# Kernel optimization log

Hardware: AMD Instinct MI355X
Metric: run time of the kernel (lower is better)

## Reference

```python
import jax, jax.numpy as jnp
import numpy as np

NUM_ROUTERS = 8
K = 2
IN_DIM = 384
HID = 64
TEMP = 1.0
AUX_COEF = 0.05
EPS = 1e-12


def _l2norm(v, axis=-1):
    n = jnp.sqrt(jnp.sum(v * v, axis=axis, keepdims=True))
    return v / jnp.maximum(n, EPS)


def setup_inputs() -> dict:
    key = jax.random.key(0)
    ks = jax.random.split(key, 10)
    B, E = 8192, 1024
    s = 1.0 / np.sqrt(IN_DIM)
    return {
        "x": jax.random.normal(ks[0], (B, IN_DIM), jnp.float32),
        "reasoning_embeddings": jax.random.normal(ks[1], (E, IN_DIM), jnp.float32),
        "random_num": jax.random.uniform(ks[2], (B, 1), jnp.float32),
        "gate_w": jax.random.normal(ks[3], (IN_DIM, NUM_ROUTERS), jnp.float32) * s,
        "gate_b": jnp.zeros((NUM_ROUTERS,), jnp.float32),
        "Uw": jax.random.normal(ks[4], (NUM_ROUTERS, IN_DIM, HID), jnp.float32) * s,
        "Ub": jnp.zeros((NUM_ROUTERS, HID), jnp.float32),
        "Vw": jax.random.normal(ks[5], (NUM_ROUTERS, IN_DIM, HID), jnp.float32) * s,
        "Vb": jnp.zeros((NUM_ROUTERS, HID), jnp.float32),
    }


def reference(x, reasoning_embeddings, random_num, gate_w, gate_b, Uw, Ub, Vw, Vb):
    B = x.shape[0]
    # gate
    logits = x @ gate_w + gate_b                              # [B, R]
    probs = jax.nn.softmax(logits, axis=-1)
    topk_vals, topk_idxs = jax.lax.top_k(logits, K)           # [B, K]
    topk_mask = jax.nn.one_hot(topk_idxs, NUM_ROUTERS).sum(axis=1)  # [B, R]
    aux_loss = NUM_ROUTERS * (probs.mean(0) * topk_mask.mean(0)).sum() * AUX_COEF

    # all routers, batched (replaces the per-(i,j) python loop)
    xu = _l2norm(jnp.einsum("bd,rdh->rbh", x, Uw) + Ub[:, None, :])          # [R, B, H]
    ev = _l2norm(jnp.einsum("ed,rdh->reh", reasoning_embeddings, Vw) + Vb[:, None, :])  # [R, E, H]
    scores = jnp.einsum("rbh,reh->rbe", xu, ev)               # [R, B, E]
    all_out = jax.nn.softmax(scores / TEMP, axis=-1)          # [R, B, E]

    # gather top-k experts per sample
    all_out_b = jnp.transpose(all_out, (1, 0, 2))             # [B, R, E]
    router_outputs = jnp.take_along_axis(all_out_b, topk_idxs[:, :, None], axis=1)  # [B, K, E]

    gate_weights = jax.nn.softmax(topk_vals, axis=-1)[:, :, None]  # [B, K, 1]
    rea_probs = jnp.sum(router_outputs * gate_weights, axis=1)     # [B, E]

    # categorical sampling via inverse-CDF
    scores_cumsum = jnp.cumsum(rea_probs, axis=1)
    selected_index = jnp.argmax((scores_cumsum > random_num).astype(jnp.float32), axis=1)  # [B]
    log_probs = jnp.log(rea_probs[jnp.arange(B), selected_index])[:, None]  # [B, 1]
    return selected_index, log_probs, aux_loss
```

## Files before the change

### kernel.cpp

```cpp
#include <hip/hip_runtime.h>
#include <math.h>

#define B 8192
#define E 1024
#define D 384
#define H 64
#define R 8
#define NCHUNK 16
#define CHUNK_E 64
#define NPOS 16896
#define NROW 25088

#define WS_COUNTS   0u
#define WS_CURSORS  32u
#define WS_PS       64u
#define WS_TOP2     256u
#define WS_GW       65792u
#define WS_POSMAP   131328u
#define WS_LIST     196864u
#define WS_EVN      264448u
#define WS_XUN      2361600u
#define WS_C        6686976u
#define WS_BUFA     7768320u
#define WS_BUFB     14190848u

__global__ __launch_bounds__(256) void k_gate(
    const float* __restrict__ x, const float* __restrict__ gate_w,
    const float* __restrict__ gate_b, int2* __restrict__ top2,
    float2* __restrict__ gwv, int* __restrict__ counts, float* __restrict__ ps)
{
  __shared__ __align__(16) float gwT[R * 388];
  __shared__ float psl[R];
  __shared__ int   cl[R];
  int tid = threadIdx.x;
  for (int idx = tid; idx < D * R; idx += 256) {
    int k = idx >> 3, r = idx & 7;
    gwT[r * 388 + k] = gate_w[idx];
  }
  if (tid < R) { psl[tid] = 0.f; cl[tid] = 0; }
  __syncthreads();

  int l = tid & 63;
  int r = tid & 7;
  int b = blockIdx.x * 32 + (tid >> 3);
  float acc = gate_b[r];
  const float4* x4 = (const float4*)(x + (size_t)b * D);
  const float*  gr = gwT + r * 388;
#pragma unroll 4
  for (int q = 0; q < 96; ++q) {
    float4 xv = x4[q];
    float4 gv = *(const float4*)&gr[q * 4];
    acc = fmaf(xv.x, gv.x, acc);
    acc = fmaf(xv.y, gv.y, acc);
    acc = fmaf(xv.z, gv.z, acc);
    acc = fmaf(xv.w, gv.w, acc);
  }
  float lv[R];
#pragma unroll
  for (int rr = 0; rr < R; ++rr) lv[rr] = __shfl(acc, (l & ~7) + rr);
  int i0 = 0; float v0 = lv[0];
#pragma unroll
  for (int rr = 1; rr < R; ++rr) if (lv[rr] > v0) { v0 = lv[rr]; i0 = rr; }
  int i1 = (i0 == 0) ? 1 : 0; float v1 = lv[i1];
#pragma unroll
  for (int rr = 0; rr < R; ++rr)
    if (rr != i0 && lv[rr] > v1) { v1 = lv[rr]; i1 = rr; }
  float se = 0.f;
#pragma unroll
  for (int rr = 0; rr < R; ++rr) se += expf(lv[rr] - v0);
  float p = expf(acc - v0) / se;
  if (r == 0) {
    float e10 = expf(v1 - v0);
    top2[b] = make_int2(i0, i1);
    gwv[b]  = make_float2(1.f / (1.f + e10), e10 / (1.f + e10));
  }
  float pa = p;
  int   ca = (r == i0 ? 1 : 0) + (r == i1 ? 1 : 0);
#pragma unroll
  for (int m = 8; m < 64; m <<= 1) {
    pa += __shfl_xor(pa, m);
    ca += __shfl_xor(ca, m);
  }
  if (l < 8) { atomicAdd(&psl[r], pa); atomicAdd(&cl[r], ca); }
  __syncthreads();
  if (tid < R) { atomicAdd(&ps[tid], psl[tid]); atomicAdd(&counts[tid], cl[tid]); }
}

__global__ __launch_bounds__(256) void k_scatter(
    const int2* __restrict__ top2, const int* __restrict__ counts,
    const float* __restrict__ ps, int* __restrict__ cursors,
    int* __restrict__ list, int2* __restrict__ posmap, float* __restrict__ out_aux)
{
  __shared__ int lc[R];
  __shared__ int lbase[R];
  __shared__ int offs[R];
  int tid = threadIdx.x;
  if (tid < R) lc[tid] = 0;
  __syncthreads();
  if (tid == 0) {
    int o = 0;
    for (int r2 = 0; r2 < R; ++r2) { offs[r2] = o; o += (min(counts[r2], B) + 63) & ~63; }
  }
  __syncthreads();
  int b = min(blockIdx.x * 256 + tid, B - 1);
  int2 t = top2[b];
  t.x &= 7; t.y &= 7;
  int p0 = atomicAdd(&lc[t.x], 1);
  int p1 = atomicAdd(&lc[t.y], 1);
  __syncthreads();
  if (tid < R) lbase[tid] = atomicAdd(&cursors[tid], lc[tid]);
  __syncthreads();
  int i0 = min(offs[t.x] + lbase[t.x] + p0, NPOS - 1);
  int i1 = min(offs[t.y] + lbase[t.y] + p1, NPOS - 1);
  list[i0] = b * 2 + 0;
  list[i1] = b * 2 + 1;
  posmap[b] = make_int2(i0, i1);
  if (blockIdx.x == 0 && tid == 0) {
    float s = 0.f;
    for (int r2 = 0; r2 < R; ++r2)
      s += (ps[r2] / (float)B) * ((float)min(counts[r2], B) / (float)B);
    out_aux[0] = (float)R * s * 0.05f;
  }
}

__global__ __launch_bounds__(256) void k_projgemm(
    const float* __restrict__ re, const float* __restrict__ x,
    const float* __restrict__ Vw, const float* __restrict__ Uw,
    const int* __restrict__ list, const int* __restrict__ counts,
    float* __restrict__ bufA, float* __restrict__ bufB)
{
  __shared__ __align__(16) float At[64 * 64];
  __shared__ __align__(16) float Wt[64 * 64];
  int tid = threadIdx.x;
  int bid = blockIdx.x;
  int tile = bid >> 1, ks = bid & 1;
  int row0 = tile * 64;

  const float* Wsrc;
  if (row0 < 8192) {
    Wsrc = Vw + (size_t)(row0 >> 10) * (D * H);
  } else {
    int pos0 = row0 - 8192;
    int r = 0, baseq = 0;
    for (int rr = 0; rr < R; ++rr) {
      if (pos0 >= baseq) r = rr;
      baseq += (min(counts[rr], B) + 63) & ~63;
    }
    Wsrc = Uw + (size_t)r * (D * H);
  }

  int srow = tid & 63, sq = tid >> 6;
  const float* arow;
  if (row0 < 8192) {
    arow = re + (size_t)((row0 + srow) & 1023) * D;
  } else {
    int pos = row0 - 8192 + srow;
    int gl = list[min(pos, NPOS - 1)];
    gl = min(max(gl, 0), 2 * B - 1);
    arow = x + (size_t)(gl >> 1) * D;
  }
  int wk = tid >> 2, wc = tid & 3;
  int rg = tid >> 4, hg = tid & 15;

  float acc[4][4];
#pragma unroll
  for (int i = 0; i < 4; ++i)
#pragma unroll
    for (int j = 0; j < 4; ++j) acc[i][j] = 0.f;

  for (int kt = 0; kt < 3; ++kt) {
    int kb = ks * 192 + kt * 64;
    __syncthreads();
#pragma unroll
    for (int q = 0; q < 4; ++q) {
      float4 v = *(const float4*)&arow[kb + sq * 16 + q * 4];
      int k0 = sq * 16 + q * 4;
      At[(k0 + 0) * 64 + srow] = v.x;
      At[(k0 + 1) * 64 + srow] = v.y;
      At[(k0 + 2) * 64 + srow] = v.z;
      At[(k0 + 3) * 64 + srow] = v.w;
    }
    const float* wrow = Wsrc + (size_t)(kb + wk) * H;
#pragma unroll
    for (int q = 0; q < 4; ++q) {
      float4 v = *(const float4*)&wrow[(wc * 4 + q) * 4];
      *(float4*)&Wt[wk * 64 + (wc * 4 + q) * 4] = v;
    }
    __syncthreads();
#pragma unroll 8
    for (int k = 0; k < 64; ++k) {
      float4 a4 = *(const float4*)&At[k * 64 + rg * 4];
      float4 w4 = *(const float4*)&Wt[k * 64 + hg * 4];
      const float* ap = (const float*)&a4;
      const float* wp = (const float*)&w4;
#pragma unroll
      for (int i = 0; i < 4; ++i)
#pragma unroll
        for (int j = 0; j < 4; ++j) acc[i][j] = fmaf(ap[i], wp[j], acc[i][j]);
    }
  }
  float* dst = (ks ? bufB : bufA) + (size_t)row0 * H;
#pragma unroll
  for (int i = 0; i < 4; ++i) {
    float4 o;
    o.x = acc[i][0]; o.y = acc[i][1]; o.z = acc[i][2]; o.w = acc[i][3];
    *(float4*)&dst[(rg * 4 + i) * H + hg * 4] = o;
  }
}

__global__ __launch_bounds__(256) void k_projfin(
    const float* __restrict__ bufA, const float* __restrict__ bufB,
    const float* __restrict__ Vb, const float* __restrict__ Ub,
    const int* __restrict__ counts, float* __restrict__ evnT,
    float* __restrict__ xunP)
{
  int tid = threadIdx.x;
  int lane = tid & 63;
  int row0 = blockIdx.x * 32 + (tid >> 6) * 8;
  bool isE = row0 < 8192;
  int r = 0;
  if (isE) {
    r = row0 >> 10;
  } else {
    int pos0 = row0 - 8192;
    int baseq = 0;
    for (int rr = 0; rr < R; ++rr) {
      if (pos0 >= baseq) r = rr;
      baseq += (min(counts[rr], B) + 63) & ~63;
    }
  }
  float bias = isE ? Vb[r * H + lane] : Ub[r * H + lane];
#pragma unroll
  for (int i = 0; i < 8; ++i) {
    int row = row0 + i;
    float s = bufA[(size_t)row * H + lane] + bufB[(size_t)row * H + lane] + bias;
    float ss = s * s;
#pragma unroll
    for (int m = 1; m < 64; m <<= 1) ss += __shfl_xor(ss, m);
    float v = s / fmaxf(sqrtf(ss), 1e-12f);
    if (isE) evnT[(size_t)(r * 64 + lane) * 1024 + (row & 1023)] = v;
    else     xunP[(size_t)(row - 8192) * H + lane] = v;
  }
}

__global__ __launch_bounds__(256) void k_pass1(
    const float* __restrict__ evnT, const float* __restrict__ xunP,
    const int* __restrict__ counts, float* __restrict__ C)
{
  __shared__ __align__(16) float Xt[64 * 128];
  __shared__ __align__(16) float Et[64 * 132];
  __shared__ int cntL[R];
  int tid = threadIdx.x;
  if (tid < R) cntL[tid] = min(counts[tid], B);
  __syncthreads();

  int bid = blockIdx.x;
  int et    = bid & 7;
  int stile = (bid >> 3) & 63;
  int r     = bid >> 9;
  int cnt = cntL[r];
  if (cnt <= 0 || stile * 128 >= cnt) return;
  int off = 0;
  for (int rr = 0; rr < r; ++rr) off += (cntL[rr] + 63) & ~63;
  off += stile * 128;
  int n = min(128, cnt - stile * 128);
  int ebase = et * 128;

  {
    int row = tid >> 1;
    int rc  = min(row, n - 1);
    const float4* src = (const float4*)(xunP + (size_t)(off + rc) * H);
    int hq0 = (tid & 1) * 8;
#pragma unroll
    for (int q = 0; q < 8; ++q) {
      float4 v = src[hq0 + q];
      int h = (hq0 + q) * 4;
      Xt[(h + 0) * 128 + row] = v.x;
      Xt[(h + 1) * 128 + row] = v.y;
      Xt[(h + 2) * 128 + row] = v.z;
      Xt[(h + 3) * 128 + row] = v.w;
    }
  }
  {
#pragma unroll
    for (int q = 0; q < 8; ++q) {
      int idx = tid + 256 * q;
      int h = idx >> 5, e4 = idx & 31;
      float4 v = *(const float4*)(evnT + (size_t)(r * 64 + h) * 1024 + ebase + e4 * 4);
      *(float4*)&Et[h * 132 + e4 * 4] = v;
    }
  }
  __syncthreads();

  int sg = tid >> 4, egr = tid & 15;
  float acc[8][8];
#pragma unroll
  for (int i = 0; i < 8; ++i)
#pragma unroll
    for (int j = 0; j < 8; ++j) acc[i][j] = 0.f;

#pragma unroll 4
  for (int k = 0; k < 64; ++k) {
    float4 xa = *(const float4*)&Xt[k * 128 + sg * 8];
    float4 xb = *(const float4*)&Xt[k * 128 + sg * 8 + 4];
    float4 ea = *(const float4*)&Et[k * 132 + egr * 4];
    float4 eb = *(const float4*)&Et[k * 132 + 64 + egr * 4];
    const float* pa = (const float*)&xa;
    const float* pb = (const float*)&xb;
    const float* qa = (const float*)&ea;
    const float* qb = (const float*)&eb;
#pragma unroll
    for (int i = 0; i < 4; ++i)
#pragma unroll
      for (int j = 0; j < 4; ++j) {
        acc[i][j]         = fmaf(pa[i], qa[j], acc[i][j]);
        acc[i][j + 4]     = fmaf(pa[i], qb[j], acc[i][j + 4]);
        acc[i + 4][j]     = fmaf(pb[i], qa[j], acc[i + 4][j]);
        acc[i + 4][j + 4] = fmaf(pb[i], qb[j], acc[i + 4][j + 4]);
      }
  }

#pragma unroll
  for (int i = 0; i < 8; ++i) {
    float cA = expf(acc[i][0]) + expf(acc[i][1]) + expf(acc[i][2]) + expf(acc[i][3]);
    float cB = expf(acc[i][4]) + expf(acc[i][5]) + expf(acc[i][6]) + expf(acc[i][7]);
#pragma unroll
    for (int m = 1; m < 16; m <<= 1) {
      cA += __shfl_xor(cA, m);
      cB += __shfl_xor(cB, m);
    }
    int s = sg * 8 + i;
    if (egr == 0 && s < n) {
      C[(size_t)(off + s) * NCHUNK + et * 2]     = cA;
      C[(size_t)(off + s) * NCHUNK + et * 2 + 1] = cB;
    }
  }
}

__global__ __launch_bounds__(256) void k_pass2(
    const float* __restrict__ evnT, const float* __restrict__ xunP,
    const float* __restrict__ C, const int2* __restrict__ top2,
    const int2* __restrict__ posmap, const float2* __restrict__ gwv,
    const float* __restrict__ rnd, float* __restrict__ out)
{
  int tid = threadIdx.x;
  int lane = tid & 63;
  int b = blockIdx.x * 4 + (tid >> 6);
  if (b >= B) return;
  int2 t2 = top2[b];
  t2.x &= 7; t2.y &= 7;
  int2 pm = posmap[b];
  pm.x = min(max(pm.x, 0), NPOS - 1);
  pm.y = min(max(pm.y, 0), NPOS - 1);
  float2 gw = gwv[b];
  float rv = rnd[b];

  const float4* C04 = (const float4*)(C + (size_t)pm.x * NCHUNK);
  const float4* C14 = (const float4*)(C + (size_t)pm.y * NCHUNK);
  float c0[NCHUNK], c1[NCHUNK];
#pragma unroll
  for (int q = 0; q < 4; ++q) {
    float4 v0 = C04[q], v1 = C14[q];
    c0[q*4+0]=v0.x; c0[q*4+1]=v0.y; c0[q*4+2]=v0.z; c0[q*4+3]=v0.w;
    c1[q*4+0]=v1.x; c1[q*4+1]=v1.y; c1[q*4+2]=v1.z; c1[q*4+3]=v1.w;
  }
  float S0 = 0.f, S1 = 0.f;
#pragma unroll
  for (int j = 0; j < NCHUNK; ++j) { S0 += c0[j]; S1 += c1[j]; }
  float a0 = gw.x / S0, a1 = gw.y / S1;
  int cstar = -1; float prefix = 0.f; float run = 0.f;
#pragma unroll
  for (int j = 0; j < NCHUNK; ++j) {
    float nrun = run + (c0[j] * a0 + c1[j] * a1);
    if (cstar < 0 && nrun > rv) { cstar = j; prefix = run; }
    run = nrun;
  }
  float rtgt = rv;
  if (cstar < 0) { cstar = 0; prefix = 0.f; rtgt = -1.0f; }

  float xu0 = xunP[(size_t)pm.x * H + lane];
  float xu1 = xunP[(size_t)pm.y * H + lane];
  const float* E0 = evnT + (size_t)t2.x * 64 * 1024 + cstar * CHUNK_E + lane;
  const float* E1 = evnT + (size_t)t2.y * 64 * 1024 + cstar * CHUNK_E + lane;
  float d0 = 0.f, d1 = 0.f;
#pragma unroll 16
  for (int h = 0; h < 64; ++h) {
    float w0 = __shfl(xu0, h);
    float w1 = __shfl(xu1, h);
    d0 = fmaf(E0[(size_t)h * 1024], w0, d0);
    d1 = fmaf(E1[(size_t)h * 1024], w1, d1);
  }
  float rea = expf(d0) * a0 + expf(d1) * a1;
  float sc = rea;
#pragma unroll
  for (int d = 1; d < 64; d <<= 1) {
    float o = __shfl_up(sc, d);
    if (lane >= d) sc += o;
  }
  float cum = prefix + sc;
  unsigned long long m2 = __ballot(cum > rtgt);
  int estar = (m2 == 0ull) ? 63 : (int)__builtin_ctzll(m2);
  float p = __shfl(rea, estar);
  if (lane == 0) {
    int sel = cstar * CHUNK_E + estar;
    out[b]     = (float)sel;
    out[B + b] = logf(p);
  }
}

extern "C" void kernel_launch(void* const* d_in, const int* in_sizes, int n_in,
                              void* d_out, int out_size, void* d_ws, size_t ws_size,
                              hipStream_t stream)
{
  (void)in_sizes; (void)n_in; (void)out_size; (void)ws_size;
  const float* x      = (const float*)d_in[0];
  const float* re     = (const float*)d_in[1];
  const float* rnd    = (const float*)d_in[2];
  const float* gate_w = (const float*)d_in[3];
  const float* gate_b = (const float*)d_in[4];
  const float* Uw     = (const float*)d_in[5];
  const float* Ub     = (const float*)d_in[6];
  const float* Vw     = (const float*)d_in[7];
  const float* Vb     = (const float*)d_in[8];
  char* ws = (char*)d_ws;
  int*    counts  = (int*)(ws + WS_COUNTS);
  int*    cursors = (int*)(ws + WS_CURSORS);
  float*  ps      = (float*)(ws + WS_PS);
  int2*   top2    = (int2*)(ws + WS_TOP2);
  float2* gwv     = (float2*)(ws + WS_GW);
  int2*   posmap  = (int2*)(ws + WS_POSMAP);
  int*    list    = (int*)(ws + WS_LIST);
  float*  evnT    = (float*)(ws + WS_EVN);
  float*  xunP    = (float*)(ws + WS_XUN);
  float*  Cc      = (float*)(ws + WS_C);
  float*  bufA    = (float*)(ws + WS_BUFA);
  float*  bufB    = (float*)(ws + WS_BUFB);
  float* out = (float*)d_out;

  hipMemsetAsync(ws, 0, 256, stream);
  k_gate    <<<256,  256, 0, stream>>>(x, gate_w, gate_b, top2, gwv, counts, ps);
  k_scatter <<<32,   256, 0, stream>>>(top2, counts, ps, cursors, list, posmap, out + 2 * B);
  k_projgemm<<<784,  256, 0, stream>>>(re, x, Vw, Uw, list, counts, bufA, bufB);
  k_projfin <<<784,  256, 0, stream>>>(bufA, bufB, Vb, Ub, counts, evnT, xunP);
  k_pass1   <<<4096, 256, 0, stream>>>(evnT, xunP, counts, Cc);
  k_pass2   <<<2048, 256, 0, stream>>>(evnT, xunP, Cc, top2, posmap, gwv, rnd, out);
}
```

Baseline: 180.7 us.

## Fuse x-projection normalization into pass kernels and enlarge projection GEMM tiles

```diff
diff --git a/kernel.cpp b/kernel.cpp
--- a/kernel.cpp
+++ b/kernel.cpp
@@ -8,8 +8,8 @@
 #define R 8
 #define NCHUNK 16
 #define CHUNK_E 64
-#define NPOS 16896
-#define NROW 25088
+#define NPOS 17408
+#define NROW 25600
 
 #define WS_COUNTS   0u
 #define WS_CURSORS  32u
@@ -18,11 +18,10 @@
 #define WS_GW       65792u
 #define WS_POSMAP   131328u
 #define WS_LIST     196864u
-#define WS_EVN      264448u
-#define WS_XUN      2361600u
-#define WS_C        6686976u
-#define WS_BUFA     7768320u
-#define WS_BUFB     14190848u
+#define WS_EVN      266496u
+#define WS_C        2363648u
+#define WS_BUFA     3477760u
+#define WS_BUFB     10031360u
 
 __global__ __launch_bounds__(256) void k_gate(
     const float* __restrict__ x, const float* __restrict__ gate_w,
@@ -99,7 +98,7 @@
   __syncthreads();
   if (tid == 0) {
     int o = 0;
-    for (int r2 = 0; r2 < R; ++r2) { offs[r2] = o; o += (min(counts[r2], B) + 63) & ~63; }
+    for (int r2 = 0; r2 < R; ++r2) { offs[r2] = o; o += (min(counts[r2], B) + 127) & ~127; }
   }
   __syncthreads();
   int b = min(blockIdx.x * 256 + tid, B - 1);
@@ -123,113 +122,110 @@
   }
 }
 
-__global__ __launch_bounds__(256) void k_projgemm(
+__global__ __launch_bounds__(128) void k_projgemm(
     const float* __restrict__ re, const float* __restrict__ x,
     const float* __restrict__ Vw, const float* __restrict__ Uw,
     const int* __restrict__ list, const int* __restrict__ counts,
     float* __restrict__ bufA, float* __restrict__ bufB)
 {
-  __shared__ __align__(16) float At[64 * 64];
+  __shared__ __align__(16) float At[64 * 128];
   __shared__ __align__(16) float Wt[64 * 64];
   int tid = threadIdx.x;
   int bid = blockIdx.x;
   int tile = bid >> 1, ks = bid & 1;
-  int row0 = tile * 64;
-
+
+  int srow = tid;
   const float* Wsrc;
-  if (row0 < 8192) {
-    Wsrc = Vw + (size_t)(row0 >> 10) * (D * H);
+  const float* arow;
+  int rowg0;
+  if (tile < 64) {
+    int r = tile >> 3;
+    rowg0 = tile * 128;
+    Wsrc = Vw + (size_t)r * (D * H);
+    arow = re + (size_t)((tile * 128 & 1023) + srow) * D;
   } else {
-    int pos0 = row0 - 8192;
-    int r = 0, baseq = 0;
+    int pos0 = (tile - 64) * 128;
+    int tot = 0, r = 0;
     for (int rr = 0; rr < R; ++rr) {
-      if (pos0 >= baseq) r = rr;
-      baseq += (min(counts[rr], B) + 63) & ~63;
-    }
+      int seg = (min(counts[rr], B) + 127) & ~127;
+      if (pos0 >= tot) r = rr;
+      tot += seg;
+    }
+    if (pos0 >= tot) return;
+    rowg0 = 8192 + pos0;
     Wsrc = Uw + (size_t)r * (D * H);
-  }
-
-  int srow = tid & 63, sq = tid >> 6;
-  const float* arow;
-  if (row0 < 8192) {
-    arow = re + (size_t)((row0 + srow) & 1023) * D;
-  } else {
-    int pos = row0 - 8192 + srow;
-    int gl = list[min(pos, NPOS - 1)];
+    int gl = list[min(pos0 + srow, NPOS - 1)];
     gl = min(max(gl, 0), 2 * B - 1);
     arow = x + (size_t)(gl >> 1) * D;
   }
-  int wk = tid >> 2, wc = tid & 3;
-  int rg = tid >> 4, hg = tid & 15;
-
-  float acc[4][4];
-#pragma unroll
-  for (int i = 0; i < 4; ++i)
-#pragma unroll
-    for (int j = 0; j < 4; ++j) acc[i][j] = 0.f;
+
+  int sg = tid >> 3, hg = tid & 7;
+  float acc[8][8];
+#pragma unroll
+  for (int i = 0; i < 8; ++i)
+#pragma unroll
+    for (int j = 0; j < 8; ++j) acc[i][j] = 0.f;
 
   for (int kt = 0; kt < 3; ++kt) {
     int kb = ks * 192 + kt * 64;
     __syncthreads();
 #pragma unroll
-    for (int q = 0; q < 4; ++q) {
-      float4 v = *(const float4*)&arow[kb + sq * 16 + q * 4];
-      int k0 = sq * 16 + q * 4;
-      At[(k0 + 0) * 64 + srow] = v.x;
-      At[(k0 + 1) * 64 + srow] = v.y;
-      At[(k0 + 2) * 64 + srow] = v.z;
-      At[(k0 + 3) * 64 + srow] = v.w;
-    }
-    const float* wrow = Wsrc + (size_t)(kb + wk) * H;
-#pragma unroll
-    for (int q = 0; q < 4; ++q) {
-      float4 v = *(const float4*)&wrow[(wc * 4 + q) * 4];
-      *(float4*)&Wt[wk * 64 + (wc * 4 + q) * 4] = v;
+    for (int q = 0; q < 16; ++q) {
+      float4 v = *(const float4*)&arow[kb + q * 4];
+      At[(q * 4 + 0) * 128 + srow] = v.x;
+      At[(q * 4 + 1) * 128 + srow] = v.y;
+      At[(q * 4 + 2) * 128 + srow] = v.z;
+      At[(q * 4 + 3) * 128 + srow] = v.w;
+    }
+#pragma unroll
+    for (int q = 0; q < 8; ++q) {
+      int idx = tid + 128 * q;
+      int k = idx >> 4, h4 = idx & 15;
+      *(float4*)&Wt[k * 64 + h4 * 4] = *(const float4*)&Wsrc[(size_t)(kb + k) * H + h4 * 4];
     }
     __syncthreads();
 #pragma unroll 8
     for (int k = 0; k < 64; ++k) {
-      float4 a4 = *(const float4*)&At[k * 64 + rg * 4];
-      float4 w4 = *(const float4*)&Wt[k * 64 + hg * 4];
-      const float* ap = (const float*)&a4;
-      const float* wp = (const float*)&w4;
+      float4 xa = *(const float4*)&At[k * 128 + sg * 4];
+      float4 xb = *(const float4*)&At[k * 128 + 64 + sg * 4];
+      float4 wa = *(const float4*)&Wt[k * 64 + hg * 4];
+      float4 wb = *(const float4*)&Wt[k * 64 + 32 + hg * 4];
+      const float* pa = (const float*)&xa;
+      const float* pb = (const float*)&xb;
+      const float* qa = (const float*)&wa;
+      const float* qb = (const float*)&wb;
 #pragma unroll
       for (int i = 0; i < 4; ++i)
 #pragma unroll
-        for (int j = 0; j < 4; ++j) acc[i][j] = fmaf(ap[i], wp[j], acc[i][j]);
-    }
-  }
-  float* dst = (ks ? bufB : bufA) + (size_t)row0 * H;
-#pragma unroll
-  for (int i = 0; i < 4; ++i) {
-    float4 o;
-    o.x = acc[i][0]; o.y = acc[i][1]; o.z = acc[i][2]; o.w = acc[i][3];
-    *(float4*)&dst[(rg * 4 + i) * H + hg * 4] = o;
-  }
-}
-
-__global__ __launch_bounds__(256) void k_projfin(
+        for (int j = 0; j < 4; ++j) {
+          acc[i][j]         = fmaf(pa[i], qa[j], acc[i][j]);
+          acc[i][j + 4]     = fmaf(pa[i], qb[j], acc[i][j + 4]);
+          acc[i + 4][j]     = fmaf(pb[i], qa[j], acc[i + 4][j]);
+          acc[i + 4][j + 4] = fmaf(pb[i], qb[j], acc[i + 4][j + 4]);
+        }
+    }
+  }
+  float* dst = (ks ? bufB : bufA) + (size_t)rowg0 * H;
+#pragma unroll
+  for (int i = 0; i < 8; ++i) {
+    int rl = (i < 4) ? (sg * 4 + i) : (64 + sg * 4 + i - 4);
+    float4 o0, o1;
+    o0.x = acc[i][0]; o0.y = acc[i][1]; o0.z = acc[i][2]; o0.w = acc[i][3];
+    o1.x = acc[i][4]; o1.y = acc[i][5]; o1.z = acc[i][6]; o1.w = acc[i][7];
+    *(float4*)&dst[rl * H + hg * 4]      = o0;
+    *(float4*)&dst[rl * H + 32 + hg * 4] = o1;
+  }
+}
+
+__global__ __launch_bounds__(256) void k_evnfin(
     const float* __restrict__ bufA, const float* __restrict__ bufB,
-    const float* __restrict__ Vb, const float* __restrict__ Ub,
-    const int* __restrict__ counts, float* __restrict__ evnT,
-    float* __restrict__ xunP)
+    const float* __restrict__ Vb, float* __restrict__ evnT)
 {
   int tid = threadIdx.x;
   int lane = tid & 63;
   int row0 = blockIdx.x * 32 + (tid >> 6) * 8;
-  bool isE = row0 < 8192;
-  int r = 0;
-  if (isE) {
-    r = row0 >> 10;
-  } else {
-    int pos0 = row0 - 8192;
-    int baseq = 0;
-    for (int rr = 0; rr < R; ++rr) {
-      if (pos0 >= baseq) r = rr;
-      baseq += (min(counts[rr], B) + 63) & ~63;
-    }
-  }
-  float bias = isE ? Vb[r * H + lane] : Ub[r * H + lane];
+  int r = row0 >> 10;
+  float bias = Vb[r * H + lane];
 #pragma unroll
   for (int i = 0; i < 8; ++i) {
     int row = row0 + i;
@@ -238,17 +234,17 @@
 #pragma unroll
     for (int m = 1; m < 64; m <<= 1) ss += __shfl_xor(ss, m);
     float v = s / fmaxf(sqrtf(ss), 1e-12f);
-    if (isE) evnT[(size_t)(r * 64 + lane) * 1024 + (row & 1023)] = v;
-    else     xunP[(size_t)(row - 8192) * H + lane] = v;
+    evnT[(size_t)(r * 64 + lane) * 1024 + (row & 1023)] = v;
   }
 }
 
 __global__ __launch_bounds__(256) void k_pass1(
-    const float* __restrict__ evnT, const float* __restrict__ xunP,
+    const float* __restrict__ evnT, const float* __restrict__ bufA,
+    const float* __restrict__ bufB, const float* __restrict__ Ub,
     const int* __restrict__ counts, float* __restrict__ C)
 {
   __shared__ __align__(16) float Xt[64 * 128];
-  __shared__ __align__(16) float Et[64 * 132];
+  __shared__ __align__(16) float Et[64 * 128];
   __shared__ int cntL[R];
   int tid = threadIdx.x;
   if (tid < R) cntL[tid] = min(counts[tid], B);
@@ -261,33 +257,41 @@
   int cnt = cntL[r];
   if (cnt <= 0 || stile * 128 >= cnt) return;
   int off = 0;
-  for (int rr = 0; rr < r; ++rr) off += (cntL[rr] + 63) & ~63;
+  for (int rr = 0; rr < r; ++rr) off += (cntL[rr] + 127) & ~127;
   off += stile * 128;
   int n = min(128, cnt - stile * 128);
   int ebase = et * 128;
 
   {
-    int row = tid >> 1;
+    int row = tid >> 1, half = tid & 1;
     int rc  = min(row, n - 1);
-    const float4* src = (const float4*)(xunP + (size_t)(off + rc) * H);
-    int hq0 = (tid & 1) * 8;
+    const float4* pA = (const float4*)(bufA + (size_t)(8192 + off + rc) * H) + half * 8;
+    const float4* pB = (const float4*)(bufB + (size_t)(8192 + off + rc) * H) + half * 8;
+    const float4* pU = (const float4*)(Ub + r * H) + half * 8;
+    float v[32]; float ss = 0.f;
 #pragma unroll
     for (int q = 0; q < 8; ++q) {
-      float4 v = src[hq0 + q];
-      int h = (hq0 + q) * 4;
-      Xt[(h + 0) * 128 + row] = v.x;
-      Xt[(h + 1) * 128 + row] = v.y;
-      Xt[(h + 2) * 128 + row] = v.z;
-      Xt[(h + 3) * 128 + row] = v.w;
-    }
+      float4 a = pA[q], bq = pB[q], u = pU[q];
+      float4 w;
+      w.x = a.x + bq.x + u.x; w.y = a.y + bq.y + u.y;
+      w.z = a.z + bq.z + u.z; w.w = a.w + bq.w + u.w;
+      v[q*4+0] = w.x; v[q*4+1] = w.y; v[q*4+2] = w.z; v[q*4+3] = w.w;
+      ss = fmaf(w.x, w.x, ss); ss = fmaf(w.y, w.y, ss);
+      ss = fmaf(w.z, w.z, ss); ss = fmaf(w.w, w.w, ss);
+    }
+    ss += __shfl_xor(ss, 1);
+    float rn = 1.f / fmaxf(sqrtf(ss), 1e-12f);
+#pragma unroll
+    for (int q = 0; q < 32; ++q)
+      Xt[(half * 32 + q) * 128 + row] = v[q] * rn;
   }
   {
 #pragma unroll
     for (int q = 0; q < 8; ++q) {
       int idx = tid + 256 * q;
       int h = idx >> 5, e4 = idx & 31;
-      float4 v = *(const float4*)(evnT + (size_t)(r * 64 + h) * 1024 + ebase + e4 * 4);
-      *(float4*)&Et[h * 132 + e4 * 4] = v;
+      *(float4*)&Et[h * 128 + e4 * 4] =
+          *(const float4*)(evnT + (size_t)(r * 64 + h) * 1024 + ebase + e4 * 4);
     }
   }
   __syncthreads();
@@ -301,10 +305,10 @@
 
 #pragma unroll 4
   for (int k = 0; k < 64; ++k) {
-    float4 xa = *(const float4*)&Xt[k * 128 + sg * 8];
-    float4 xb = *(const float4*)&Xt[k * 128 + sg * 8 + 4];
-    float4 ea = *(const float4*)&Et[k * 132 + egr * 4];
-    float4 eb = *(const float4*)&Et[k * 132 + 64 + egr * 4];
+    float4 xa = *(const float4*)&Xt[k * 128 + sg * 4];
+    float4 xb = *(const float4*)&Xt[k * 128 + 64 + sg * 4];
+    float4 ea = *(const float4*)&Et[k * 128 + egr * 4];
+    float4 eb = *(const float4*)&Et[k * 128 + 64 + egr * 4];
     const float* pa = (const float*)&xa;
     const float* pb = (const float*)&xb;
     const float* qa = (const float*)&ea;
@@ -329,7 +333,7 @@
       cA += __shfl_xor(cA, m);
       cB += __shfl_xor(cB, m);
     }
-    int s = sg * 8 + i;
+    int s = (i < 4) ? (sg * 4 + i) : (64 + sg * 4 + i - 4);
     if (egr == 0 && s < n) {
       C[(size_t)(off + s) * NCHUNK + et * 2]     = cA;
       C[(size_t)(off + s) * NCHUNK + et * 2 + 1] = cB;
@@ -338,7 +342,8 @@
 }
 
 __global__ __launch_bounds__(256) void k_pass2(
-    const float* __restrict__ evnT, const float* __restrict__ xunP,
+    const float* __restrict__ evnT, const float* __restrict__ bufA,
+    const float* __restrict__ bufB, const float* __restrict__ Ub,
     const float* __restrict__ C, const int2* __restrict__ top2,
     const int2* __restrict__ posmap, const float2* __restrict__ gwv,
     const float* __restrict__ rnd, float* __restrict__ out)
@@ -378,8 +383,16 @@
   float rtgt = rv;
   if (cstar < 0) { cstar = 0; prefix = 0.f; rtgt = -1.0f; }
 
-  float xu0 = xunP[(size_t)pm.x * H + lane];
-  float xu1 = xunP[(size_t)pm.y * H + lane];
+  float v0x = bufA[(size_t)(8192 + pm.x) * H + lane] +
+              bufB[(size_t)(8192 + pm.x) * H + lane] + Ub[t2.x * H + lane];
+  float v1x = bufA[(size_t)(8192 + pm.y) * H + lane] +
+              bufB[(size_t)(8192 + pm.y) * H + lane] + Ub[t2.y * H + lane];
+  float s0 = v0x * v0x, s1 = v1x * v1x;
+#pragma unroll
+  for (int m = 1; m < 64; m <<= 1) { s0 += __shfl_xor(s0, m); s1 += __shfl_xor(s1, m); }
+  float xu0 = v0x / fmaxf(sqrtf(s0), 1e-12f);
+  float xu1 = v1x / fmaxf(sqrtf(s1), 1e-12f);
+
   const float* E0 = evnT + (size_t)t2.x * 64 * 1024 + cstar * CHUNK_E + lane;
   const float* E1 = evnT + (size_t)t2.y * 64 * 1024 + cstar * CHUNK_E + lane;
   float d0 = 0.f, d1 = 0.f;
@@ -431,7 +444,6 @@
   int2*   posmap  = (int2*)(ws + WS_POSMAP);
   int*    list    = (int*)(ws + WS_LIST);
   float*  evnT    = (float*)(ws + WS_EVN);
-  float*  xunP    = (float*)(ws + WS_XUN);
   float*  Cc      = (float*)(ws + WS_C);
   float*  bufA    = (float*)(ws + WS_BUFA);
   float*  bufB    = (float*)(ws + WS_BUFB);
@@ -440,8 +452,8 @@
   hipMemsetAsync(ws, 0, 256, stream);
   k_gate    <<<256,  256, 0, stream>>>(x, gate_w, gate_b, top2, gwv, counts, ps);
   k_scatter <<<32,   256, 0, stream>>>(top2, counts, ps, cursors, list, posmap, out + 2 * B);
-  k_projgemm<<<784,  256, 0, stream>>>(re, x, Vw, Uw, list, counts, bufA, bufB);
-  k_projfin <<<784,  256, 0, stream>>>(bufA, bufB, Vb, Ub, counts, evnT, xunP);
-  k_pass1   <<<4096, 256, 0, stream>>>(evnT, xunP, counts, Cc);
-  k_pass2   <<<2048, 256, 0, stream>>>(evnT, xunP, Cc, top2, posmap, gwv, rnd, out);
-}
+  k_projgemm<<<400,  128, 0, stream>>>(re, x, Vw, Uw, list, counts, bufA, bufB);
+  k_evnfin  <<<256,  256, 0, stream>>>(bufA, bufB, Vb, evnT);
+  k_pass1   <<<4096, 256, 0, stream>>>(evnT, bufA, bufB, Ub, counts, Cc);
+  k_pass2   <<<2048, 256, 0, stream>>>(evnT, bufA, bufB, Ub, Cc, top2, posmap, gwv, rnd, out);
+}
```

Measured after the change: 194.4 us. 1.08x slower.
